# Performance work log

Hardware: AMD Instinct MI355X
Metric: run time of the kernel (lower is better)

Reference implementation:

```python
import jax, jax.numpy as jnp
import numpy as np

B, S, H, NH = 8, 1024, 768, 12
I = 3072
HD = H // NH  # 64


def setup_inputs() -> dict:
    key = jax.random.key(0)
    ks = jax.random.split(key, 6)
    w = lambda k, shape: jax.random.normal(k, shape, jnp.float32) * 0.02
    return {
        "x": jax.random.normal(ks[0], (B, S, H), jnp.float32),
        "ln1_g": jnp.ones((H,), jnp.float32),
        "ln1_b": jnp.zeros((H,), jnp.float32),
        "qkv_w": w(ks[1], (H, 3 * H)),
        "qkv_b": jnp.zeros((3 * H,), jnp.float32),
        "proj_w": w(ks[2], (H, H)),
        "proj_b": jnp.zeros((H,), jnp.float32),
        "ln2_g": jnp.ones((H,), jnp.float32),
        "ln2_b": jnp.zeros((H,), jnp.float32),
        "fc1_w": w(ks[3], (H, I)),
        "fc1_b": jnp.zeros((I,), jnp.float32),
        "fc2_w": w(ks[4], (I, H)),
        "fc2_b": jnp.zeros((H,), jnp.float32),
    }


def _layernorm(x, g, b, eps=1e-5):
    m = x.mean(-1, keepdims=True)
    v = x.var(-1, keepdims=True)  # biased variance, matches torch LayerNorm
    return (x - m) * jax.lax.rsqrt(v + eps) * g + b


def _new_gelu(x):
    c = np.float32(np.sqrt(2.0 / np.pi))
    return 0.5 * x * (1.0 + jnp.tanh(c * (x + 0.044715 * x * x * x)))


def reference(x, ln1_g, ln1_b, qkv_w, qkv_b, proj_w, proj_b,
              ln2_g, ln2_b, fc1_w, fc1_b, fc2_w, fc2_b):
    # --- attention sublayer (pre-LN) ---
    h = _layernorm(x, ln1_g, ln1_b)                     # [B,S,H]
    qkv = h @ qkv_w + qkv_b                             # [B,S,3H]
    q, k, v = jnp.split(qkv, 3, axis=-1)
    q = q.reshape(B, S, NH, HD).transpose(0, 2, 1, 3)   # [B,NH,S,HD]
    k = k.reshape(B, S, NH, HD).transpose(0, 2, 1, 3)
    v = v.reshape(B, S, NH, HD).transpose(0, 2, 1, 3)
    scores = jnp.einsum('bhtd,bhsd->bhts', q, k) / np.float32(np.sqrt(HD))
    probs = jax.nn.softmax(scores, axis=-1)             # [B,NH,S,S]
    attn = jnp.einsum('bhts,bhsd->bhtd', probs, v)      # [B,NH,S,HD]
    attn = attn.transpose(0, 2, 1, 3).reshape(B, S, H)
    attn = attn @ proj_w + proj_b
    x = x + attn
    # --- MLP sublayer (pre-LN) ---
    h2 = _layernorm(x, ln2_g, ln2_b)
    m = _new_gelu(h2 @ fc1_w + fc1_b) @ fc2_w + fc2_b
    return x + m
```

## Files before the change

### kernel.cpp

```cpp
#include <hip/hip_runtime.h>
#include <hip/hip_bf16.h>


typedef __attribute__((ext_vector_type(8))) short bf16x8;
typedef __attribute__((ext_vector_type(4))) float f32x4;
typedef const __attribute__((address_space(3))) char* lds_cp;

#define MFMA16(a, b, c) __builtin_amdgcn_mfma_f32_16x16x32_bf16((a), (b), (c), 0, 0, 0)

#define DSR(dst, addr, off) \
    asm volatile("ds_read_b128 %0, %1 offset:" #off : "=v"(dst) : "v"(addr))
#define WAITV4 asm volatile("s_waitcnt vmcnt(4)" ::: "memory")
#define WAITV0 asm volatile("s_waitcnt vmcnt(0)" ::: "memory")
#define WAITLG asm volatile("s_waitcnt lgkmcnt(0)" ::: "memory")
#define SCHEDB __builtin_amdgcn_sched_barrier(0)
#define CVTPK(d, lo, hi) \
    asm("v_cvt_pk_bf16_f32 %0, %1, %2" : "=v"(d) : "v"(lo), "v"(hi))

__device__ inline short f2bf(float x) {
    __hip_bfloat16 h = __float2bfloat16(x);
    return *reinterpret_cast<short*>(&h);
}

__device__ inline void gload_lds16(const void* g, void* lds) {
    __builtin_amdgcn_global_load_lds(
        (const __attribute__((address_space(1))) unsigned int*)g,
        (__attribute__((address_space(3))) unsigned int*)lds,
        16, 0, 0);
}

__global__ __launch_bounds__(256) void transpose_w(
    const float* __restrict__ W, short* __restrict__ Wt, int K, int N) {
    __shared__ float tile[32][33];
    const int tx = threadIdx.x & 31, ty = threadIdx.x >> 5;
    const int n0 = blockIdx.x * 32, k0 = blockIdx.y * 32;
#pragma unroll
    for (int i = 0; i < 4; ++i)
        tile[ty + i * 8][tx] = W[(size_t)(k0 + ty + i * 8) * N + n0 + tx];
    __syncthreads();
#pragma unroll
    for (int i = 0; i < 4; ++i)
        Wt[(size_t)(n0 + ty + i * 8) * K + k0 + tx] = f2bf(tile[tx][ty + i * 8]);
}

__global__ __launch_bounds__(256) void ln_k(
    const float* __restrict__ x, const float* __restrict__ g,
    const float* __restrict__ b, short* __restrict__ out) {
    const int row = blockIdx.x;
    const int tid = threadIdx.x;
    const float* xr = x + (size_t)row * 768;
    float v[3];
    float s = 0.f, sq = 0.f;
#pragma unroll
    for (int i = 0; i < 3; ++i) {
        v[i] = xr[tid + i * 256];
        s += v[i];
        sq += v[i] * v[i];
    }
#pragma unroll
    for (int off = 32; off >= 1; off >>= 1) {
        s += __shfl_xor(s, off);
        sq += __shfl_xor(sq, off);
    }
    __shared__ float ss[4], ssq[4];
    const int wid = tid >> 6;
    if ((tid & 63) == 0) { ss[wid] = s; ssq[wid] = sq; }
    __syncthreads();
    s = ss[0] + ss[1] + ss[2] + ss[3];
    sq = ssq[0] + ssq[1] + ssq[2] + ssq[3];
    const float mean = s * (1.0f / 768.0f);
    const float var = sq * (1.0f / 768.0f) - mean * mean;
    const float rstd = rsqrtf(var + 1e-5f);
    short* outr = out + (size_t)row * 768;
#pragma unroll
    for (int i = 0; i < 3; ++i) {
        const int c = tid + i * 256;
        outr[c] = f2bf((v[i] - mean) * rstd * g[c] + b[c]);
    }
}

enum { MODE_BF16 = 0, MODE_QKV = 1, MODE_F32RES = 2, MODE_GELU = 3 };

template <int MODE>
__global__ __launch_bounds__(256) void gemm3p(
    const short* __restrict__ A, const short* __restrict__ Wt,
    const float* __restrict__ bias, const float* __restrict__ resid,
    float* __restrict__ outf, short* __restrict__ outh,
    short* __restrict__ Qo, short* __restrict__ Ko, short* __restrict__ Vto,
    int M, int N, int K) {
    __shared__ __attribute__((aligned(128))) short Al[3][4096];
    __shared__ __attribute__((aligned(128))) short Bl[3][4096];
    const int tid = threadIdx.x;
    const int lane = tid & 63;
    const int w = tid >> 6;
    const int wm = w >> 1, wn = w & 1;
    const int m0 = blockIdx.x * 128, n0 = blockIdx.y * 128;

    f32x4 acc[4][4] = {};

    const int srow = tid >> 2;
    const int scol = ((tid & 3) * 8) ^ (((tid >> 2) & 3) << 3);
    const short* Abase = A + (size_t)(m0 + srow) * K + scol;
    const short* Bbase = Wt + (size_t)(n0 + srow) * K + scol;
    const size_t K64 = (size_t)K * 64;
    short* const AlF = &Al[0][0];
    short* const BlF = &Bl[0][0];

    auto stageT = [&](int boS, int k0s) {
        gload_lds16(Abase + k0s,       AlF + boS + w * 512);
        gload_lds16(Abase + K64 + k0s, AlF + boS + 2048 + w * 512);
        gload_lds16(Bbase + k0s,       BlF + boS + w * 512);
        gload_lds16(Bbase + K64 + k0s, BlF + boS + 2048 + w * 512);
    };

    const int lrow = lane & 15;
    const int lcolswz = ((lane >> 4) * 16) ^ ((lane & 3) << 4);
    const int aoff = wm * 4096 + lrow * 64 + lcolswz;
    const int boff = wn * 4096 + lrow * 64 + lcolswz;
    const lds_cp AlB = (lds_cp)AlF;
    const lds_cp BlB = (lds_cp)BlF;

    const int NT = K >> 5;

    stageT(0, 0);
    stageT(4096, 32);
    WAITV4;
    SCHEDB;
    __builtin_amdgcn_s_barrier();

    int bo = 0, bo1 = 8192, bo2 = 16384;
    for (int t = 0; t < NT; ++t) {
        const lds_cp Ab = AlB + (bo + aoff);
        const lds_cp Bb = BlB + (bo + boff);
        bf16x8 av0, av1, av2, av3, bv0, bv1, bv2, bv3;
        DSR(av0, Ab, 0);
        DSR(av1, Ab, 1024);
        DSR(av2, Ab, 2048);
        DSR(av3, Ab, 3072);
        DSR(bv0, Bb, 0);
        DSR(bv1, Bb, 1024);
        DSR(bv2, Bb, 2048);
        DSR(bv3, Bb, 3072);

        int ts = t + 2;
        if (ts > NT - 1) ts = NT - 1;
        stageT(bo2 >> 1, ts << 5);
        WAITV4;
        SCHEDB;
        __builtin_amdgcn_s_barrier();
        WAITLG;
        SCHEDB;

        __builtin_amdgcn_s_setprio(1);
        {
            bf16x8 av[4] = {av0, av1, av2, av3};
            bf16x8 bv[4] = {bv0, bv1, bv2, bv3};
#pragma unroll
            for (int mi = 0; mi < 4; ++mi)
#pragma unroll
                for (int ni = 0; ni < 4; ++ni)
                    acc[mi][ni] = MFMA16(av[mi], bv[ni], acc[mi][ni]);
        }
        __builtin_amdgcn_s_setprio(0);
        __builtin_amdgcn_s_barrier();

        const int tmp = bo; bo = bo1; bo1 = bo2; bo2 = tmp;
    }
    WAITV0;

#pragma unroll
    for (int mi = 0; mi < 4; ++mi) {
#pragma unroll
        for (int ni = 0; ni < 4; ++ni) {
#pragma unroll
            for (int r = 0; r < 4; ++r) {
                const int row = m0 + wm * 64 + mi * 16 + (lane >> 4) * 4 + r;
                const int col = n0 + wn * 64 + ni * 16 + (lane & 15);
                float v = acc[mi][ni][r] + bias[col];
                if constexpr (MODE == MODE_BF16) {
                    outh[(size_t)row * N + col] = f2bf(v);
                } else if constexpr (MODE == MODE_GELU) {
                    const float u = 0.7978845608028654f * (v + 0.044715f * v * v * v);
                    const float gl = v / (1.0f + __expf(-2.0f * u));
                    outh[(size_t)row * N + col] = f2bf(gl);
                } else if constexpr (MODE == MODE_F32RES) {
                    outf[(size_t)row * N + col] = v + resid[(size_t)row * N + col];
                } else {
                    const int bb = row >> 10, s = row & 1023;
                    if (col < 768) {
                        const int hh = col >> 6, d = col & 63;
                        Qo[(((size_t)(bb * 12 + hh)) * 1024 + s) * 64 + d] = f2bf(v * 0.125f);
                    } else if (col < 1536) {
                        const int c2 = col - 768;
                        const int hh = c2 >> 6, d = c2 & 63;
                        Ko[(((size_t)(bb * 12 + hh)) * 1024 + s) * 64 + d] = f2bf(v);
                    } else {
                        const int c2 = col - 1536;
                        const int hh = c2 >> 6, d = c2 & 63;
                        Vto[(((size_t)(bb * 12 + hh)) * 64 + d) * 1024 + s] = f2bf(v);
                    }
                }
            }
        }
    }
}

__global__ __launch_bounds__(256) void attn_k(
    const short* __restrict__ Q, const short* __restrict__ Kg,
    const short* __restrict__ Vtg, short* __restrict__ out) {
    __shared__ __attribute__((aligned(128))) short Kl[2][64 * 64];
    __shared__ __attribute__((aligned(128))) short Vl[2][64 * 64];
    __shared__ __attribute__((aligned(128))) short Pl[4][16 * 64];
    const int tid = threadIdx.x, lane = tid & 63, w = tid >> 6;
    const int swz = (blockIdx.x & 7) * 192 + (blockIdx.x >> 3);
    const int qt = swz & 15, bh = swz >> 4;
    const int b = bh / 12, h = bh % 12;
    const int q0 = qt * 64 + w * 16;
    const int l15 = lane & 15, g = lane >> 4;

    bf16x8 aq[2];
    const short* Qb = Q + ((size_t)bh * 1024 + q0) * 64;
#pragma unroll
    for (int kk = 0; kk < 2; ++kk)
        aq[kk] = *(const bf16x8*)&Qb[(size_t)l15 * 64 + kk * 32 + g * 8];

    float m_run = -1e30f, l_run = 0.f;
    f32x4 o[4] = {};

    const short* Kb = Kg + (size_t)bh * 1024 * 64;
    const short* Vb = Vtg + (size_t)bh * 64 * 1024;

    const int srr = tid >> 3;
    const int spp = (tid & 7) * 8;
    const int ssc = spp ^ ((srr & 7) << 3);
    auto stage = [&](int buf, int kv0) {
        gload_lds16(Kb + (size_t)(kv0 + srr) * 64 + ssc,        &Kl[buf][w * 512]);
        gload_lds16(Kb + (size_t)(kv0 + 32 + srr) * 64 + ssc,   &Kl[buf][2048 + w * 512]);
        gload_lds16(Vb + (size_t)srr * 1024 + kv0 + ssc,        &Vl[buf][w * 512]);
        gload_lds16(Vb + (size_t)(srr + 32) * 1024 + kv0 + ssc, &Vl[buf][2048 + w * 512]);
    };

    stage(0, 0);
    __syncthreads();

    int buf = 0;
    for (int t = 0; t < 16; ++t) {
        const lds_cp KB = (lds_cp)&Kl[buf][0];
        const lds_cp VB = (lds_cp)&Vl[buf][0];

        bf16x8 kb[4][2];
#pragma unroll
        for (int nk = 0; nk < 4; ++nk) {
            const int R = nk * 16 + l15;
            const int c0 = (g * 8) ^ ((R & 7) << 3);
            const lds_cp a0 = KB + R * 128 + c0 * 2;
            const lds_cp a1 = KB + R * 128 + (c0 ^ 32) * 2;
            DSR(kb[nk][0], a0, 0);
            DSR(kb[nk][1], a1, 0);
        }

        if (t < 15) stage(buf ^ 1, (t + 1) * 64);

        WAITLG;
        SCHEDB;

        f32x4 sc4[4];
#pragma unroll
        for (int nk = 0; nk < 4; ++nk) {
            f32x4 z = {};
            z = MFMA16(kb[nk][0], aq[0], z);
            z = MFMA16(kb[nk][1], aq[1], z);
            sc4[nk] = z;
        }

        float ml = sc4[0][0];
#pragma unroll
        for (int nk = 0; nk < 4; ++nk)
#pragma unroll
            for (int r = 0; r < 4; ++r) ml = fmaxf(ml, sc4[nk][r]);
        ml = fmaxf(ml, __shfl_xor(ml, 16));
        ml = fmaxf(ml, __shfl_xor(ml, 32));
        const float mn = fmaxf(m_run, ml);
        const float alpha = __expf(m_run - mn);
        m_run = mn;
        float padd[4][4];
        float rsum = 0.f;
#pragma unroll
        for (int nk = 0; nk < 4; ++nk)
#pragma unroll
            for (int r = 0; r < 4; ++r) {
                padd[nk][r] = __expf(sc4[nk][r] - mn);
                rsum += padd[nk][r];
            }
        rsum += __shfl_xor(rsum, 16);
        rsum += __shfl_xor(rsum, 32);
        l_run = l_run * alpha + rsum;
#pragma unroll
        for (int dn = 0; dn < 4; ++dn) o[dn] *= alpha;

#pragma unroll
        for (int nk = 0; nk < 4; ++nk) {
            unsigned u0, u1;
            CVTPK(u0, padd[nk][0], padd[nk][1]);
            CVTPK(u1, padd[nk][2], padd[nk][3]);
            const int cc = (nk * 16 + g * 4) ^ ((l15 & 7) << 3);
            uint2 uv; uv.x = u0; uv.y = u1;
            *reinterpret_cast<uint2*>(&Pl[w][l15 * 64 + cc]) = uv;
        }
        bf16x8 pa[2];
#pragma unroll
        for (int kk = 0; kk < 2; ++kk)
            pa[kk] = *(const bf16x8*)&Pl[w][l15 * 64 + ((kk * 32 + g * 8) ^ ((l15 & 7) << 3))];

        bf16x8 vb[4][2];
#pragma unroll
        for (int dn = 0; dn < 4; ++dn) {
            const int R = dn * 16 + l15;
            const int c0 = (g * 8) ^ ((R & 7) << 3);
            const lds_cp a0 = VB + R * 128 + c0 * 2;
            const lds_cp a1 = VB + R * 128 + (c0 ^ 32) * 2;
            DSR(vb[dn][0], a0, 0);
            DSR(vb[dn][1], a1, 0);
        }
        WAITLG;
        SCHEDB;

#pragma unroll
        for (int dn = 0; dn < 4; ++dn) {
            o[dn] = MFMA16(vb[dn][0], pa[0], o[dn]);
            o[dn] = MFMA16(vb[dn][1], pa[1], o[dn]);
        }

        __syncthreads();
        buf ^= 1;
    }

    const float rl = __builtin_amdgcn_rcpf(l_run);
    short* orow = out + ((size_t)(b * 1024) + q0 + l15) * 768 + h * 64;
#pragma unroll
    for (int dn = 0; dn < 4; ++dn) {
        unsigned u0, u1;
        const float v0 = o[dn][0] * rl, v1 = o[dn][1] * rl;
        const float v2 = o[dn][2] * rl, v3 = o[dn][3] * rl;
        CVTPK(u0, v0, v1);
        CVTPK(u1, v2, v3);
        uint2 uv; uv.x = u0; uv.y = u1;
        *reinterpret_cast<uint2*>(&orow[dn * 16 + g * 4]) = uv;
    }
}

extern "C" void kernel_launch(void* const* d_in, const int* in_sizes, int n_in,
                              void* d_out, int out_size, void* d_ws, size_t ws_size,
                              hipStream_t stream) {
    const float* x      = (const float*)d_in[0];
    const float* ln1_g  = (const float*)d_in[1];
    const float* ln1_b  = (const float*)d_in[2];
    const float* qkv_w  = (const float*)d_in[3];
    const float* qkv_b  = (const float*)d_in[4];
    const float* proj_w = (const float*)d_in[5];
    const float* proj_b = (const float*)d_in[6];
    const float* ln2_g  = (const float*)d_in[7];
    const float* ln2_b  = (const float*)d_in[8];
    const float* fc1_w  = (const float*)d_in[9];
    const float* fc1_b  = (const float*)d_in[10];
    const float* fc2_w  = (const float*)d_in[11];
    const float* fc2_b  = (const float*)d_in[12];
    float* outp = (float*)d_out;

    char* ws = (char*)d_ws;
    size_t off = 0;
    auto alloc = [&](size_t bytes) {
        char* p = ws + off;
        off = (off + bytes + 255) & ~(size_t)255;
        return p;
    };
    short* wt_qkv  = (short*)alloc(2304ull * 768 * 2);
    short* wt_proj = (short*)alloc(768ull * 768 * 2);
    short* wt_fc1  = (short*)alloc(3072ull * 768 * 2);
    short* wt_fc2  = (short*)alloc(768ull * 3072 * 2);
    short* hbuf    = (short*)alloc(8192ull * 768 * 2);
    short* Qb      = (short*)alloc(8192ull * 768 * 2);
    short* Kbuf    = (short*)alloc(8192ull * 768 * 2);
    short* Vtb     = (short*)alloc(8192ull * 768 * 2);
    short* attnb   = (short*)alloc(8192ull * 768 * 2);
    float* x2      = (float*)alloc(8192ull * 768 * 4);
    short* mfc     = Qb;
    (void)ws_size; (void)in_sizes; (void)n_in; (void)out_size;

    transpose_w<<<dim3(2304 / 32, 768 / 32), 256, 0, stream>>>(qkv_w, wt_qkv, 768, 2304);
    transpose_w<<<dim3(768 / 32, 768 / 32), 256, 0, stream>>>(proj_w, wt_proj, 768, 768);
    transpose_w<<<dim3(3072 / 32, 768 / 32), 256, 0, stream>>>(fc1_w, wt_fc1, 768, 3072);
    transpose_w<<<dim3(768 / 32, 3072 / 32), 256, 0, stream>>>(fc2_w, wt_fc2, 3072, 768);

    ln_k<<<8192, 256, 0, stream>>>(x, ln1_g, ln1_b, hbuf);
    gemm3p<MODE_QKV><<<dim3(64, 18), 256, 0, stream>>>(
        hbuf, wt_qkv, qkv_b, nullptr, nullptr, nullptr, Qb, Kbuf, Vtb, 8192, 2304, 768);
    attn_k<<<1536, 256, 0, stream>>>(Qb, Kbuf, Vtb, attnb);
    gemm3p<MODE_F32RES><<<dim3(64, 6), 256, 0, stream>>>(
        attnb, wt_proj, proj_b, x, x2, nullptr, nullptr, nullptr, nullptr, 8192, 768, 768);

    ln_k<<<8192, 256, 0, stream>>>(x2, ln2_g, ln2_b, hbuf);
    gemm3p<MODE_GELU><<<dim3(64, 24), 256, 0, stream>>>(
        hbuf, wt_fc1, fc1_b, nullptr, nullptr, mfc, nullptr, nullptr, nullptr, 8192, 3072, 768);
    gemm3p<MODE_F32RES><<<dim3(64, 6), 256, 0, stream>>>(
        mfc, wt_fc2, fc2_b, x2, outp, nullptr, nullptr, nullptr, nullptr, 8192, 768, 3072);
}
```

Measured before the change: 280.3 us.

## Double-buffer LDS fragment registers to overlap ds_reads with MFMA in GEMM

Restructures the GEMM main loop so the LDS reads for the next K-step go into a second register set while MFMAs run on the current set. The loop is unrolled by two with ping-pong registers, and one barrier per step replaces two. The goal is to hide LDS read latency behind matrix math. In exchange it raises VGPR pressure, which can reduce occupancy. The triple-buffer stage indexing with one fewer barrier also risks races, and the unroll by two assumes NT is even.

```diff
diff --git a/kernel.cpp b/kernel.cpp
--- a/kernel.cpp
+++ b/kernel.cpp
@@ -9,7 +9,7 @@
 #define MFMA16(a, b, c) __builtin_amdgcn_mfma_f32_16x16x32_bf16((a), (b), (c), 0, 0, 0)
 
 #define DSR(dst, addr, off) \
-    asm volatile("ds_read_b128 %0, %1 offset:" #off : "=v"(dst) : "v"(addr))
+    asm volatile("ds_read_b128 %0, %1 offset:" #off : "=&v"(dst) : "v"(addr))
 #define WAITV4 asm volatile("s_waitcnt vmcnt(4)" ::: "memory")
 #define WAITV0 asm volatile("s_waitcnt vmcnt(0)" ::: "memory")
 #define WAITLG asm volatile("s_waitcnt lgkmcnt(0)" ::: "memory")
@@ -121,51 +121,67 @@
     const lds_cp BlB = (lds_cp)BlF;
 
     const int NT = K >> 5;
+    const int last = NT - 1;
+
+    bf16x8 ra0, ra1, ra2, ra3, rb0, rb1, rb2, rb3;
+    bf16x8 sa0, sa1, sa2, sa3, sb0, sb1, sb2, sb3;
 
     stageT(0, 0);
     stageT(4096, 32);
     WAITV4;
     SCHEDB;
     __builtin_amdgcn_s_barrier();
-
-    int bo = 0, bo1 = 8192, bo2 = 16384;
-    for (int t = 0; t < NT; ++t) {
-        const lds_cp Ab = AlB + (bo + aoff);
-        const lds_cp Bb = BlB + (bo + boff);
-        bf16x8 av0, av1, av2, av3, bv0, bv1, bv2, bv3;
-        DSR(av0, Ab, 0);
-        DSR(av1, Ab, 1024);
-        DSR(av2, Ab, 2048);
-        DSR(av3, Ab, 3072);
-        DSR(bv0, Bb, 0);
-        DSR(bv1, Bb, 1024);
-        DSR(bv2, Bb, 2048);
-        DSR(bv3, Bb, 3072);
-
-        int ts = t + 2;
-        if (ts > NT - 1) ts = NT - 1;
-        stageT(bo2 >> 1, ts << 5);
-        WAITV4;
-        SCHEDB;
-        __builtin_amdgcn_s_barrier();
-        WAITLG;
-        SCHEDB;
-
-        __builtin_amdgcn_s_setprio(1);
-        {
-            bf16x8 av[4] = {av0, av1, av2, av3};
-            bf16x8 bv[4] = {bv0, bv1, bv2, bv3};
-#pragma unroll
-            for (int mi = 0; mi < 4; ++mi)
-#pragma unroll
-                for (int ni = 0; ni < 4; ++ni)
-                    acc[mi][ni] = MFMA16(av[mi], bv[ni], acc[mi][ni]);
-        }
-        __builtin_amdgcn_s_setprio(0);
-        __builtin_amdgcn_s_barrier();
-
-        const int tmp = bo; bo = bo1; bo1 = bo2; bo2 = tmp;
-    }
+    {
+        const lds_cp Ab = AlB + aoff;
+        const lds_cp Bb = BlB + boff;
+        DSR(ra0, Ab, 0); DSR(ra1, Ab, 1024); DSR(ra2, Ab, 2048); DSR(ra3, Ab, 3072);
+        DSR(rb0, Bb, 0); DSR(rb1, Bb, 1024); DSR(rb2, Bb, 2048); DSR(rb3, Bb, 3072);
+    }
+    stageT(8192, 64);
+    WAITLG;
+    SCHEDB;
+
+    int rdo = 8192, sto = 0;
+    auto rot = [](int v) { return v == 16384 ? 0 : v + 8192; };
+
+#define GEMM_SUBITER(RA0,RA1,RA2,RA3,RB0,RB1,RB2,RB3, SA0,SA1,SA2,SA3,SB0,SB1,SB2,SB3, U) \
+    {                                                                                     \
+        WAITV4;                                                                           \
+        SCHEDB;                                                                           \
+        __builtin_amdgcn_s_barrier();                                                     \
+        {                                                                                 \
+            int tr = (U) + 1; if (tr > last) tr = last;                                   \
+            const int rb_ = (tr % 3) * 8192;                                              \
+            const lds_cp Ab = AlB + rb_ + aoff;                                           \
+            const lds_cp Bb = BlB + rb_ + boff;                                           \
+            DSR(SA0, Ab, 0); DSR(SA1, Ab, 1024); DSR(SA2, Ab, 2048); DSR(SA3, Ab, 3072);  \
+            DSR(SB0, Bb, 0); DSR(SB1, Bb, 1024); DSR(SB2, Bb, 2048); DSR(SB3, Bb, 3072);  \
+            int ts = (U) + 3; if (ts > last) ts = last;                                   \
+            stageT((((U) + 3) % 3) * 4096, ts << 5);                                      \
+        }                                                                                 \
+        __builtin_amdgcn_s_setprio(1);                                                    \
+        {                                                                                 \
+            bf16x8 av[4] = {RA0, RA1, RA2, RA3};                                          \
+            bf16x8 bv[4] = {RB0, RB1, RB2, RB3};                                          \
+            _Pragma("unroll")                                                             \
+            for (int mi = 0; mi < 4; ++mi)                                                \
+                _Pragma("unroll")                                                         \
+                for (int ni = 0; ni < 4; ++ni)                                            \
+                    acc[mi][ni] = MFMA16(av[mi], bv[ni], acc[mi][ni]);                    \
+        }                                                                                 \
+        __builtin_amdgcn_s_setprio(0);                                                    \
+        WAITLG;                                                                           \
+        SCHEDB;                                                                           \
+    }
+
+    for (int t = 0; t < NT; t += 2) {
+        GEMM_SUBITER(ra0, ra1, ra2, ra3, rb0, rb1, rb2, rb3,
+                     sa0, sa1, sa2, sa3, sb0, sb1, sb2, sb3, t);
+        GEMM_SUBITER(sa0, sa1, sa2, sa3, sb0, sb1, sb2, sb3,
+                     ra0, ra1, ra2, ra3, rb0, rb1, rb2, rb3, t + 1);
+        (void)rdo; (void)sto;
+    }
+#undef GEMM_SUBITER
     WAITV0;
 
 #pragma unroll
```

Result: slower. 286.7 us (+2.3%).

## Add wide 128x256 tile GEMM for QKV and FC1 projections

Applied to the files above, without the earlier changes.

Adds a new GEMM kernel with a 128x256 output tile per block (each wave computes 64x128) and a two-stage LDS double buffer. It replaces the 128x128 triple-buffered kernel for the QKV and FC1 GEMMs and halves the grid in N. The goal is more MFMA reuse per LDS read and fewer blocks re-reading A. The cost is more accumulator registers, lower occupancy, and a shallower prefetch pipeline. The epilogue is also factored into a shared helper.

```diff
diff --git a/kernel.cpp b/kernel.cpp
--- a/kernel.cpp
+++ b/kernel.cpp
@@ -80,6 +80,137 @@
 }
 
 enum { MODE_BF16 = 0, MODE_QKV = 1, MODE_F32RES = 2, MODE_GELU = 3 };
+
+template <int MODE>
+__device__ inline void epi_store(
+    float v, int row, int col, int N,
+    const float* __restrict__ resid, float* __restrict__ outf,
+    short* __restrict__ outh, short* __restrict__ Qo,
+    short* __restrict__ Ko, short* __restrict__ Vto) {
+    if constexpr (MODE == MODE_BF16) {
+        outh[(size_t)row * N + col] = f2bf(v);
+    } else if constexpr (MODE == MODE_GELU) {
+        const float u = 0.7978845608028654f * (v + 0.044715f * v * v * v);
+        const float gl = v / (1.0f + __expf(-2.0f * u));
+        outh[(size_t)row * N + col] = f2bf(gl);
+    } else if constexpr (MODE == MODE_F32RES) {
+        outf[(size_t)row * N + col] = v + resid[(size_t)row * N + col];
+    } else {
+        const int bb = row >> 10, s = row & 1023;
+        if (col < 768) {
+            const int hh = col >> 6, d = col & 63;
+            Qo[(((size_t)(bb * 12 + hh)) * 1024 + s) * 64 + d] = f2bf(v * 0.125f);
+        } else if (col < 1536) {
+            const int c2 = col - 768;
+            const int hh = c2 >> 6, d = c2 & 63;
+            Ko[(((size_t)(bb * 12 + hh)) * 1024 + s) * 64 + d] = f2bf(v);
+        } else {
+            const int c2 = col - 1536;
+            const int hh = c2 >> 6, d = c2 & 63;
+            Vto[(((size_t)(bb * 12 + hh)) * 64 + d) * 1024 + s] = f2bf(v);
+        }
+    }
+}
+
+template <int MODE>
+__global__ __launch_bounds__(256) void gemmW(
+    const short* __restrict__ A, const short* __restrict__ Wt,
+    const float* __restrict__ bias, const float* __restrict__ resid,
+    float* __restrict__ outf, short* __restrict__ outh,
+    short* __restrict__ Qo, short* __restrict__ Ko, short* __restrict__ Vto,
+    int M, int N, int K) {
+    __shared__ __attribute__((aligned(128))) short Al[2][4096];
+    __shared__ __attribute__((aligned(128))) short Bl[2][8192];
+    const int tid = threadIdx.x;
+    const int lane = tid & 63;
+    const int w = tid >> 6;
+    const int wm = w >> 1, wn = w & 1;
+    const int m0 = blockIdx.x * 128, n0 = blockIdx.y * 256;
+
+    f32x4 acc[4][8] = {};
+
+    const int srow = tid >> 2;
+    const int scol = ((tid & 3) * 8) ^ (((tid >> 2) & 3) << 3);
+    short* const AlF = &Al[0][0];
+    short* const BlF = &Bl[0][0];
+    const short* Ab0 = A + (size_t)(m0 + srow) * K + scol;
+    const short* Bb0 = Wt + (size_t)(n0 + srow) * K + scol;
+    const size_t K64 = (size_t)K * 64;
+
+    auto stageW = [&](int p, int k0s) {
+        gload_lds16(Ab0 + k0s,            AlF + p * 4096 + w * 512);
+        gload_lds16(Ab0 + K64 + k0s,      AlF + p * 4096 + 2048 + w * 512);
+        gload_lds16(Bb0 + k0s,            BlF + p * 8192 + w * 512);
+        gload_lds16(Bb0 + K64 + k0s,      BlF + p * 8192 + 2048 + w * 512);
+        gload_lds16(Bb0 + 2 * K64 + k0s,  BlF + p * 8192 + 4096 + w * 512);
+        gload_lds16(Bb0 + 3 * K64 + k0s,  BlF + p * 8192 + 6144 + w * 512);
+    };
+
+    const int l15 = lane & 15;
+    const int lcolswz = ((lane >> 4) * 16) ^ ((lane & 3) << 4);
+    const int aoff = wm * 4096 + l15 * 64 + lcolswz;
+    const int boff = wn * 8192 + l15 * 64 + lcolswz;
+    const lds_cp AlB = (lds_cp)AlF;
+    const lds_cp BlB = (lds_cp)BlF;
+
+    const int NT = K >> 5;
+
+    stageW(0, 0);
+    WAITV0;
+    SCHEDB;
+
+    for (int t = 0; t < NT; ++t) {
+        __builtin_amdgcn_s_barrier();
+        SCHEDB;
+        const int p = t & 1;
+        const lds_cp Ap = AlB + p * 8192 + aoff;
+        const lds_cp Bp = BlB + p * 16384 + boff;
+        bf16x8 a0, a1, a2, a3, b0, b1, b2, b3, b4, b5, b6, b7;
+        DSR(a0, Ap, 0);
+        DSR(a1, Ap, 1024);
+        DSR(a2, Ap, 2048);
+        DSR(a3, Ap, 3072);
+        DSR(b0, Bp, 0);
+        DSR(b1, Bp, 1024);
+        DSR(b2, Bp, 2048);
+        DSR(b3, Bp, 3072);
+        DSR(b4, Bp, 4096);
+        DSR(b5, Bp, 5120);
+        DSR(b6, Bp, 6144);
+        DSR(b7, Bp, 7168);
+
+        if (t + 1 < NT) stageW(p ^ 1, (t + 1) << 5);
+
+        WAITLG;
+        SCHEDB;
+
+        __builtin_amdgcn_s_setprio(1);
+        {
+            bf16x8 av[4] = {a0, a1, a2, a3};
+            bf16x8 bv[8] = {b0, b1, b2, b3, b4, b5, b6, b7};
+#pragma unroll
+            for (int mi = 0; mi < 4; ++mi)
+#pragma unroll
+                for (int ni = 0; ni < 8; ++ni)
+                    acc[mi][ni] = MFMA16(av[mi], bv[ni], acc[mi][ni]);
+        }
+        __builtin_amdgcn_s_setprio(0);
+        WAITV0;
+        SCHEDB;
+    }
+
+#pragma unroll
+    for (int mi = 0; mi < 4; ++mi)
+#pragma unroll
+        for (int ni = 0; ni < 8; ++ni)
+#pragma unroll
+            for (int r = 0; r < 4; ++r) {
+                const int row = m0 + wm * 64 + mi * 16 + (lane >> 4) * 4 + r;
+                const int col = n0 + wn * 128 + ni * 16 + l15;
+                epi_store<MODE>(acc[mi][ni][r] + bias[col], row, col, N,
+                                resid, outf, outh, Qo, Ko, Vto);
+            }
+}
 
 template <int MODE>
 __global__ __launch_bounds__(256) void gemm3p(
@@ -169,40 +300,16 @@
     WAITV0;
 
 #pragma unroll
-    for (int mi = 0; mi < 4; ++mi) {
-#pragma unroll
-        for (int ni = 0; ni < 4; ++ni) {
+    for (int mi = 0; mi < 4; ++mi)
+#pragma unroll
+        for (int ni = 0; ni < 4; ++ni)
 #pragma unroll
             for (int r = 0; r < 4; ++r) {
                 const int row = m0 + wm * 64 + mi * 16 + (lane >> 4) * 4 + r;
                 const int col = n0 + wn * 64 + ni * 16 + (lane & 15);
-                float v = acc[mi][ni][r] + bias[col];
-                if constexpr (MODE == MODE_BF16) {
-                    outh[(size_t)row * N + col] = f2bf(v);
-                } else if constexpr (MODE == MODE_GELU) {
-                    const float u = 0.7978845608028654f * (v + 0.044715f * v * v * v);
-                    const float gl = v / (1.0f + __expf(-2.0f * u));
-                    outh[(size_t)row * N + col] = f2bf(gl);
-                } else if constexpr (MODE == MODE_F32RES) {
-                    outf[(size_t)row * N + col] = v + resid[(size_t)row * N + col];
-                } else {
-                    const int bb = row >> 10, s = row & 1023;
-                    if (col < 768) {
-                        const int hh = col >> 6, d = col & 63;
-                        Qo[(((size_t)(bb * 12 + hh)) * 1024 + s) * 64 + d] = f2bf(v * 0.125f);
-                    } else if (col < 1536) {
-                        const int c2 = col - 768;
-                        const int hh = c2 >> 6, d = c2 & 63;
-                        Ko[(((size_t)(bb * 12 + hh)) * 1024 + s) * 64 + d] = f2bf(v);
-                    } else {
-                        const int c2 = col - 1536;
-                        const int hh = c2 >> 6, d = c2 & 63;
-                        Vto[(((size_t)(bb * 12 + hh)) * 64 + d) * 1024 + s] = f2bf(v);
-                    }
-                }
+                epi_store<MODE>(acc[mi][ni][r] + bias[col], row, col, N,
+                                resid, outf, outh, Qo, Ko, Vto);
             }
-        }
-    }
 }
 
 __global__ __launch_bounds__(256) void attn_k(
@@ -393,14 +500,14 @@
     transpose_w<<<dim3(768 / 32, 3072 / 32), 256, 0, stream>>>(fc2_w, wt_fc2, 3072, 768);
 
     ln_k<<<8192, 256, 0, stream>>>(x, ln1_g, ln1_b, hbuf);
-    gemm3p<MODE_QKV><<<dim3(64, 18), 256, 0, stream>>>(
+    gemmW<MODE_QKV><<<dim3(64, 9), 256, 0, stream>>>(
         hbuf, wt_qkv, qkv_b, nullptr, nullptr, nullptr, Qb, Kbuf, Vtb, 8192, 2304, 768);
     attn_k<<<1536, 256, 0, stream>>>(Qb, Kbuf, Vtb, attnb);
     gemm3p<MODE_F32RES><<<dim3(64, 6), 256, 0, stream>>>(
         attnb, wt_proj, proj_b, x, x2, nullptr, nullptr, nullptr, nullptr, 8192, 768, 768);
 
     ln_k<<<8192, 256, 0, stream>>>(x2, ln2_g, ln2_b, hbuf);
-    gemm3p<MODE_GELU><<<dim3(64, 24), 256, 0, stream>>>(
+    gemmW<MODE_GELU><<<dim3(64, 12), 256, 0, stream>>>(
         hbuf, wt_fc1, fc1_b, nullptr, nullptr, mfc, nullptr, nullptr, nullptr, 8192, 3072, 768);
     gemm3p<MODE_F32RES><<<dim3(64, 6), 256, 0, stream>>>(
         mfc, wt_fc2, fc2_b, x2, outp, nullptr, nullptr, nullptr, nullptr, 8192, 768, 3072);
```

Measured after the change: 327.5 us. 16.8% more time.
